# Kernel tuning notes

Measured on AMD Instinct MI355X. Metric: run time of the kernel, lower is better.

The kernel has to match this reference:

```python
import jax, jax.numpy as jnp
import numpy as np
from jax import lax

K = 9
CENTER = K // 2
EXTEND = 1.0
EPS = 1e-5
GROUPS = 16  # out_ch // 4


def conv2d(x, w, b, stride, padding):
    y = lax.conv_general_dilated(x, w, window_strides=stride, padding=padding,
                                 dimension_numbers=('NCHW', 'OIHW', 'NCHW'))
    return y + b[None, :, None, None]


def setup_inputs() -> dict:
    key = jax.random.key(0)
    ks = jax.random.split(key, 9)
    B, C, Wd, Hd, OUT = 8, 64, 128, 128, 64
    f = jax.random.normal(ks[0], (B, C, Wd, Hd), jnp.float32)
    w_off = jax.random.normal(ks[1], (2 * K, C, 3, 3), jnp.float32) * 0.05
    b_off = jax.random.normal(ks[2], (2 * K,), jnp.float32) * 0.05
    bn_gamma = 1.0 + 0.1 * jax.random.normal(ks[3], (2 * K,), jnp.float32)
    bn_beta = 0.1 * jax.random.normal(ks[4], (2 * K,), jnp.float32)
    w_dsc = jax.random.normal(ks[5], (OUT, C, K, 1), jnp.float32) * 0.05
    b_dsc = jax.random.normal(ks[6], (OUT,), jnp.float32) * 0.05
    gn_gamma = 1.0 + 0.1 * jax.random.normal(ks[7], (OUT,), jnp.float32)
    gn_beta = 0.1 * jax.random.normal(ks[8], (OUT,), jnp.float32)
    return {'f': f, 'w_off': w_off, 'b_off': b_off, 'bn_gamma': bn_gamma,
            'bn_beta': bn_beta, 'w_dsc': w_dsc, 'b_dsc': b_dsc,
            'gn_gamma': gn_gamma, 'gn_beta': gn_beta}


def _forward(f, w_off, b_off, bn_gamma, bn_beta, w_dsc, b_dsc, gn_gamma, gn_beta):
    B, C, Wd, Hd = f.shape  # module names: width=shape[2], height=shape[3]
    dt = f.dtype

    # offset branch: conv3x3 -> BatchNorm (training mode, batch stats) -> tanh
    off = conv2d(f, w_off, b_off, (1, 1), 'SAME')
    mu = off.mean(axis=(0, 2, 3), keepdims=True)
    var = off.var(axis=(0, 2, 3), keepdims=True)
    off = (off - mu) / jnp.sqrt(var + EPS)
    off = off * bn_gamma[None, :, None, None] + bn_beta[None, :, None, None]
    off = jnp.tanh(off)

    y_off = off[:, :K]  # [B,K,Wd,Hd]; x_off (off[:, K:]) unused for morph=0

    # cumulative offset scan from the center point (morph=0).
    # NOTE: endpoints 0 and K-1 keep detached raw offsets (torch detach().clone()).
    raw0 = lax.stop_gradient(y_off)
    offn = [None] * K
    offn[CENTER] = jnp.zeros_like(y_off[:, 0])
    for i in range(1, CENTER):
        offn[CENTER + i] = offn[CENTER + i - 1] + y_off[:, CENTER + i]
        offn[CENTER - i] = offn[CENTER - i + 1] + y_off[:, CENTER - i]
    offn[0] = raw0[:, 0]
    offn[K - 1] = raw0[:, K - 1]
    offn = jnp.stack(offn, axis=1)  # [B,K,Wd,Hd]

    # coordinate grids: y indexes the width axis, x the height axis
    y_new = jnp.arange(Wd, dtype=dt)[None, None, :, None] + offn * EXTEND  # [B,K,Wd,Hd]
    x_new = ((jnp.arange(K, dtype=dt) - CENTER)[None, :, None, None]
             + jnp.arange(Hd, dtype=dt)[None, None, None, :])  # [1,K,1,Hd]
    x_new = jnp.broadcast_to(x_new, (B, K, Wd, Hd))

    # layout [B, K*Wd, Hd] via (B,K,Wd,Hd) -> (B,Wd,K,Hd)
    y_s = jnp.transpose(y_new, (0, 2, 1, 3)).reshape(B, K * Wd * Hd)
    x_s = jnp.transpose(x_new, (0, 2, 1, 3)).reshape(B, K * Wd * Hd)

    # bilinear interpolation (clamped corner indices, unclamped y/x in weights)
    y0 = jnp.floor(y_s).astype(jnp.int32)
    x0 = jnp.floor(x_s).astype(jnp.int32)
    y0c = jnp.clip(y0, 0, Wd - 1)
    y1c = jnp.clip(y0 + 1, 0, Wd - 1)
    x0c = jnp.clip(x0, 0, Hd - 1)
    x1c = jnp.clip(x0 + 1, 0, Hd - 1)

    feat = jnp.transpose(f, (0, 2, 3, 1)).reshape(B, Wd * Hd, C)

    def gather(yi, xi):
        idx = (yi * Hd + xi)[:, :, None]  # [B,N,1]
        return jnp.take_along_axis(feat, idx, axis=1)  # [B,N,C]

    va0 = gather(y0c, x0c)
    vc0 = gather(y0c, x1c)
    va1 = gather(y1c, x0c)
    vc1 = gather(y1c, x1c)

    y0f, y1f = y0c.astype(dt), y1c.astype(dt)
    x0f, x1f = x0c.astype(dt), x1c.astype(dt)
    wa = ((y1f - y_s) * (x1f - x_s))[:, :, None]
    wb = ((y1f - y_s) * (x_s - x0f))[:, :, None]
    wc = ((y_s - y0f) * (x1f - x_s))[:, :, None]
    wd = ((y_s - y0f) * (x_s - x0f))[:, :, None]

    out = va0 * wa + vc0 * wb + va1 * wc + vc1 * wd  # [B,N,C]
    deformed = jnp.transpose(out.reshape(B, K * Wd, Hd, C), (0, 3, 1, 2))  # [B,C,K*Wd,Hd]

    # strided conv over the K snake points -> [B,OUT,Wd,Hd]
    x = conv2d(deformed, w_dsc, b_dsc, (K, 1), 'VALID')

    # GroupNorm + ReLU
    OUT = x.shape[1]
    xg = x.reshape(B, GROUPS, -1)
    gmu = xg.mean(axis=-1, keepdims=True)
    gvar = xg.var(axis=-1, keepdims=True)
    xg = (xg - gmu) / jnp.sqrt(gvar + EPS)
    x = xg.reshape(x.shape) * gn_gamma[None, :, None, None] + gn_beta[None, :, None, None]
    return jax.nn.relu(x)


def reference(f, w_off, b_off, bn_gamma, bn_beta, w_dsc, b_dsc, gn_gamma, gn_beta):
    return _forward(f, w_off, b_off, bn_gamma, bn_beta, w_dsc, b_dsc, gn_gamma, gn_beta)
```

## Files before the change

### kernel.cpp

```cpp
#include <hip/hip_runtime.h>

#define B_   8
#define C_   64
#define W_   128
#define H_   128
#define K_   9
#define OUT_ 64
#define NPIX (B_*W_*H_)
#define EPS_ 1e-5f

typedef __attribute__((ext_vector_type(8))) short bf16x8;
typedef __attribute__((ext_vector_type(4))) float f32x4;

#define FEATBF_OFF  0
#define XPRE_OFF    4194304
#define OFFPRE_OFF  8388608
#define OFFH_OFF    9568256
#define WT_OFF      14286848
#define WP_OFF      14305280
#define BNSTATS_OFF 14310464
#define GSTATS_OFF  14310500
#define STATS_BYTES ((18+18+256+256)*sizeof(float))

__device__ __forceinline__ unsigned pack2bf(float a, float b) {
    union { float f; unsigned u; } ua, ub;
    ua.f = a; ub.f = b;
    unsigned x = ua.u, y = ub.u;
    x += 0x7fffu + ((x >> 16) & 1u);
    y += 0x7fffu + ((y >> 16) & 1u);
    return (x >> 16) | (y & 0xffff0000u);
}
__device__ __forceinline__ float bflo(unsigned u) {
    union { unsigned u; float f; } v; v.u = u << 16; return v.f;
}
__device__ __forceinline__ float bfhi(unsigned u) {
    union { unsigned u; float f; } v; v.u = u & 0xffff0000u; return v.f;
}

__global__ __launch_bounds__(256) void k_nhwc(const float* __restrict__ f,
                                              unsigned short* __restrict__ featbf) {
    __shared__ float tile[64][65];
    int bid = blockIdx.x;
    int ht = bid & 1;
    int w  = (bid >> 1) & 127;
    int b  = bid >> 8;
    int t  = threadIdx.x;
    int lh = t & 63;
    int c0 = (t >> 6) * 16;
    const float* fp = f + (((b*64)*128 + w)*128) + ht*64 + lh;
#pragma unroll
    for (int i = 0; i < 16; i++) {
        int c = c0 + i;
        tile[c][lh] = fp[c*16384];
    }
    __syncthreads();
    int lc = t & 63;
    int h0 = (t >> 6) * 16;
    unsigned short* obf = featbf + ((size_t)((b*128 + w)*128) + ht*64)*64 + lc;
#pragma unroll
    for (int i = 0; i < 16; i++) {
        int hr = h0 + i;
        union { float f; unsigned u; } v; v.f = tile[lc][hr];
        unsigned x = v.u + 0x7fffu + ((v.u >> 16) & 1u);
        obf[(size_t)hr*64] = (unsigned short)(x >> 16);
    }
}

__global__ void k_wprep(const float* __restrict__ w_dsc, unsigned short* __restrict__ wTbf,
                        const float* __restrict__ w_off, float* __restrict__ wP) {
    int bid = blockIdx.x;
    if (bid < 144) {
        int i = bid*256 + threadIdx.x;
        if (i >= 9*64*64) return;
        int c = i & 63;
        int o = (i >> 6) & 63;
        int k = i >> 12;
        union { float f; unsigned u; } v;
        v.f = w_dsc[(o*64 + c)*9 + k];
        unsigned x = v.u + 0x7fffu + ((v.u >> 16) & 1u);
        wTbf[i] = (unsigned short)(x >> 16);
    } else {
        int i = (bid-144)*256 + threadIdx.x;
        if (i >= 64*81) return;
        int c    = i / 81;
        int rem  = i % 81;
        int dw   = rem / 27;
        int rem2 = rem % 27;
        int ck   = rem2 / 3;
        int dh   = rem2 % 3;
        wP[i] = w_off[ck*576 + c*9 + dw*3 + dh];
    }
}

__global__ __launch_bounds__(128) void k_conv_off(const float* __restrict__ f,
                                                  const float* __restrict__ wP,
                                                  float* __restrict__ off_half) {
    int t   = threadIdx.x;
    int bid = blockIdx.x;
    int b   = bid & 7;
    int w   = (bid >> 3) & 127;
    int cq  = bid >> 10;
    int h   = t;

    float em = (h == 0)   ? 0.f : 1.f;
    float ep = (h == 127) ? 0.f : 1.f;

    const float* fb = f + (size_t)b*1048576 + (size_t)(cq*16)*16384 + (size_t)w*128;
    const float* wb = wP + cq*16*81;

    float acc[9];
#pragma unroll
    for (int ck = 0; ck < 9; ck++) acc[ck] = 0.f;

#pragma unroll 4
    for (int c = 0; c < 16; c++) {
        const float* p  = fb + c*16384;
        const float* wc = wb + c*81;
#pragma unroll
        for (int dw = -1; dw <= 1; dw++) {
            int wy = w + dw;
            if ((unsigned)wy < 128u) {
                const float* q = p + dw*128;
                float v1 = q[h];
                float v0 = __shfl_up(v1, 1);
                float v2 = __shfl_down(v1, 1);
                if (t == 64) v0 = q[63];
                if (t == 63) v2 = q[64];
                v0 *= em; v2 *= ep;
                const float* ww = wc + (dw+1)*27;
#pragma unroll
                for (int ck = 0; ck < 9; ck++)
                    acc[ck] += v0*ww[ck*3] + v1*ww[ck*3+1] + v2*ww[ck*3+2];
            }
        }
    }

    float* dst = off_half + (size_t)cq*1179648;
    int pixoff = (w << 7) + h;
#pragma unroll
    for (int ck = 0; ck < 9; ck++)
        dst[((b*9 + ck) << 14) + pixoff] = acc[ck];
}

__global__ __launch_bounds__(256) void k_bn_stats(const float* __restrict__ off_half,
                                                  float* __restrict__ off_pre,
                                                  float* __restrict__ bnstats) {
    __shared__ float wred[4][2];
    int bid = blockIdx.x;
    int b  = bid / 36;
    int rem = bid % 36;
    int ck = rem / 4;
    int wq = rem % 4;
    int t  = threadIdx.x;
    int base4 = (((b*9+ck) << 14) + wq*4096) >> 2;

    const float4* h0 = (const float4*)off_half;
    const float4* h1 = (const float4*)(off_half + 1179648);
    const float4* h2 = (const float4*)(off_half + 2359296);
    const float4* h3 = (const float4*)(off_half + 3538944);
    float4* op = (float4*)off_pre;

    float s = 0.f, q = 0.f;
#pragma unroll
    for (int i = 0; i < 4; i++) {
        int idx = base4 + t + i*256;
        float4 a = h0[idx], bb = h1[idx], cc = h2[idx], dd = h3[idx];
        float4 v;
        v.x = (a.x + bb.x) + (cc.x + dd.x);
        v.y = (a.y + bb.y) + (cc.y + dd.y);
        v.z = (a.z + bb.z) + (cc.z + dd.z);
        v.w = (a.w + bb.w) + (cc.w + dd.w);
        op[idx] = v;
        s += v.x + v.y + v.z + v.w;
        q += v.x*v.x + v.y*v.y + v.z*v.z + v.w*v.w;
    }
    for (int off = 32; off; off >>= 1) {
        s += __shfl_down(s, off);
        q += __shfl_down(q, off);
    }
    if ((t & 63) == 0) { wred[t >> 6][0] = s; wred[t >> 6][1] = q; }
    __syncthreads();
    if (t == 0) atomicAdd(&bnstats[ck*2],   wred[0][0]+wred[1][0]+wred[2][0]+wred[3][0]);
    if (t == 1) atomicAdd(&bnstats[ck*2+1], wred[0][1]+wred[1][1]+wred[2][1]+wred[3][1]);
}

__global__ __launch_bounds__(256) void k_sample_dsc(const unsigned short* __restrict__ featbf,
                                                    const float* __restrict__ off_pre,
                                                    const float* __restrict__ bnstats,
                                                    const float* __restrict__ bn_gamma,
                                                    const float* __restrict__ bn_beta,
                                                    const unsigned short* __restrict__ wTbf,
                                                    const float* __restrict__ b_dsc,
                                                    unsigned short* __restrict__ xprebf,
                                                    float* __restrict__ gstats) {
    __shared__ __align__(16) unsigned char lds_samp[2][64*128];
    __shared__ __align__(16) unsigned char lds_wk[2][64*128];
    __shared__ float ynew[9][64];
    __shared__ float red[16][2];
    __shared__ float bnab[18];

    int t = threadIdx.x;
    int bid = blockIdx.x;
    int b = bid & 7, w = (bid >> 3) & 127, mh = bid >> 10;
    int hbase = mh * 64;

    if (t < 9) {
        float n    = (float)NPIX;
        float mean = bnstats[t*2] / n;
        float var  = bnstats[t*2+1] / n - mean*mean;
        float A    = bn_gamma[t] / sqrtf(var + EPS_);
        bnab[t*2]   = A;
        bnab[t*2+1] = bn_beta[t] - mean * A;
    }
    if (t < 16) { red[t][0] = 0.f; red[t][1] = 0.f; }
    __syncthreads();

    if (t < 64) {
        int h = hbase + t;
        float y[9];
#pragma unroll
        for (int ck = 0; ck < 9; ck++) {
            float v = off_pre[((b*9+ck) << 14) + (w << 7) + h];
            y[ck] = tanhf(bnab[ck*2]*v + bnab[ck*2+1]);
        }
        float ofn[9];
        ofn[4] = 0.f;
        ofn[5] = y[5]; ofn[6] = y[5]+y[6]; ofn[7] = y[5]+y[6]+y[7];
        ofn[3] = y[3]; ofn[2] = y[3]+y[2]; ofn[1] = y[3]+y[2]+y[1];
        ofn[0] = y[0]; ofn[8] = y[8];
#pragma unroll
        for (int k = 0; k < 9; k++) ynew[k][t] = (float)w + ofn[k];
    }
    __syncthreads();

    f32x4 acc[4];
#pragma unroll
    for (int ni = 0; ni < 4; ni++) {
        acc[ni][0] = 0.f; acc[ni][1] = 0.f; acc[ni][2] = 0.f; acc[ni][3] = 0.f;
    }

    int lane = t & 63, wv = t >> 6;
    int m0 = wv * 16;
    int lm = lane & 15, lk = lane >> 4;
    int hsl = t >> 2;
    int cq  = t & 3;
    const unsigned short* pbase = featbf + ((size_t)b << 20);

    uint4 sa0, sa1, sb0, sb1, wv0, wv1;
    float twa = 0.f, twc = 0.f;
    bool valid = false;

    {
        int hg = hbase + hsl;
        int x0 = 0 - 4 + hg;
        valid = (unsigned)x0 < 127u;
        if (valid) {
            float ys = ynew[0][hsl];
            int y0  = (int)floorf(ys);
            int y0c = min(max(y0, 0), 127), y1c = min(max(y0+1, 0), 127);
            twa = (float)y1c - ys; twc = ys - (float)y0c;
            const uint4* p0 = (const uint4*)(pbase + (y0c*128 + x0)*64) + cq*2;
            const uint4* p1 = (const uint4*)(pbase + (y1c*128 + x0)*64) + cq*2;
            sa0 = p0[0]; sa1 = p0[1];
            sb0 = p1[0]; sb1 = p1[1];
        }
        const uint4* src = (const uint4*)wTbf;
        wv0 = src[t]; wv1 = src[t + 256];
    }
    {
        unsigned char* dst = lds_samp[0] + hsl*128;
        int bcol0 = cq * 32;
        uint4 u0 = make_uint4(0,0,0,0), u1 = make_uint4(0,0,0,0);
        if (valid) {
            u0.x = pack2bf(bflo(sa0.x)*twa + bflo(sb0.x)*twc, bfhi(sa0.x)*twa + bfhi(sb0.x)*twc);
            u0.y = pack2bf(bflo(sa0.y)*twa + bflo(sb0.y)*twc, bfhi(sa0.y)*twa + bfhi(sb0.y)*twc);
            u0.z = pack2bf(bflo(sa0.z)*twa + bflo(sb0.z)*twc, bfhi(sa0.z)*twa + bfhi(sb0.z)*twc);
            u0.w = pack2bf(bflo(sa0.w)*twa + bflo(sb0.w)*twc, bfhi(sa0.w)*twa + bfhi(sb0.w)*twc);
            u1.x = pack2bf(bflo(sa1.x)*twa + bflo(sb1.x)*twc, bfhi(sa1.x)*twa + bfhi(sb1.x)*twc);
            u1.y = pack2bf(bflo(sa1.y)*twa + bflo(sb1.y)*twc, bfhi(sa1.y)*twa + bfhi(sb1.y)*twc);
            u1.z = pack2bf(bflo(sa1.z)*twa + bflo(sb1.z)*twc, bfhi(sa1.z)*twa + bfhi(sb1.z)*twc);
            u1.w = pack2bf(bflo(sa1.w)*twa + bflo(sb1.w)*twc, bfhi(sa1.w)*twa + bfhi(sb1.w)*twc);
        }
        *(uint4*)(dst + ((bcol0     ) ^ ((hsl & 7) << 4))) = u0;
        *(uint4*)(dst + ((bcol0 + 16) ^ ((hsl & 7) << 4))) = u1;
#pragma unroll
        for (int i = 0; i < 2; i++) {
            int ci = t + i*256;
            uint4 v = (i == 0) ? wv0 : wv1;
            int o  = ci >> 3;
            int cb = (ci & 7) << 4;
            *(uint4*)(lds_wk[0] + o*128 + (cb ^ ((o & 7) << 4))) = v;
        }
    }
    __syncthreads();

    for (int k = 0; k < 9; k++) {
        int cur = k & 1, nxt = cur ^ 1;

        if (k < 8) {
            int hg = hbase + hsl;
            int x0 = (k+1) - 4 + hg;
            valid = (unsigned)x0 < 127u;
            if (valid) {
                float ys = ynew[k+1][hsl];
                int y0  = (int)floorf(ys);
                int y0c = min(max(y0, 0), 127), y1c = min(max(y0+1, 0), 127);
                twa = (float)y1c - ys; twc = ys - (float)y0c;
                const uint4* p0 = (const uint4*)(pbase + (y0c*128 + x0)*64) + cq*2;
                const uint4* p1 = (const uint4*)(pbase + (y1c*128 + x0)*64) + cq*2;
                sa0 = p0[0]; sa1 = p0[1];
                sb0 = p1[0]; sb1 = p1[1];
            }
            const uint4* src = (const uint4*)(wTbf + ((k+1) << 12));
            wv0 = src[t]; wv1 = src[t + 256];
        }

#pragma unroll
        for (int ks = 0; ks < 2; ks++) {
            bf16x8 af, bfr[4];
            {
                int hl = m0 + lm;
                af = *(const bf16x8*)(lds_samp[cur] + hl*128 + ((ks*64 + lk*16) ^ ((hl & 7) << 4)));
            }
#pragma unroll
            for (int ni = 0; ni < 4; ni++) {
                int o = ni*16 + lm;
                bfr[ni] = *(const bf16x8*)(lds_wk[cur] + o*128 + ((ks*64 + lk*16) ^ ((o & 7) << 4)));
            }
#pragma unroll
            for (int ni = 0; ni < 4; ni++)
                acc[ni] = __builtin_amdgcn_mfma_f32_16x16x32_bf16(af, bfr[ni], acc[ni], 0, 0, 0);
        }

        if (k < 8) {
            unsigned char* dst = lds_samp[nxt] + hsl*128;
            int bcol0 = cq * 32;
            uint4 u0 = make_uint4(0,0,0,0), u1 = make_uint4(0,0,0,0);
            if (valid) {
                u0.x = pack2bf(bflo(sa0.x)*twa + bflo(sb0.x)*twc, bfhi(sa0.x)*twa + bfhi(sb0.x)*twc);
                u0.y = pack2bf(bflo(sa0.y)*twa + bflo(sb0.y)*twc, bfhi(sa0.y)*twa + bfhi(sb0.y)*twc);
                u0.z = pack2bf(bflo(sa0.z)*twa + bflo(sb0.z)*twc, bfhi(sa0.z)*twa + bfhi(sb0.z)*twc);
                u0.w = pack2bf(bflo(sa0.w)*twa + bflo(sb0.w)*twc, bfhi(sa0.w)*twa + bfhi(sb0.w)*twc);
                u1.x = pack2bf(bflo(sa1.x)*twa + bflo(sb1.x)*twc, bfhi(sa1.x)*twa + bfhi(sb1.x)*twc);
                u1.y = pack2bf(bflo(sa1.y)*twa + bflo(sb1.y)*twc, bfhi(sa1.y)*twa + bfhi(sb1.y)*twc);
                u1.z = pack2bf(bflo(sa1.z)*twa + bflo(sb1.z)*twc, bfhi(sa1.z)*twa + bfhi(sb1.z)*twc);
                u1.w = pack2bf(bflo(sa1.w)*twa + bflo(sb1.w)*twc, bfhi(sa1.w)*twa + bfhi(sb1.w)*twc);
            }
            *(uint4*)(dst + ((bcol0     ) ^ ((hsl & 7) << 4))) = u0;
            *(uint4*)(dst + ((bcol0 + 16) ^ ((hsl & 7) << 4))) = u1;
#pragma unroll
            for (int i = 0; i < 2; i++) {
                int ci = t + i*256;
                uint4 v = (i == 0) ? wv0 : wv1;
                int o  = ci >> 3;
                int cb = (ci & 7) << 4;
                *(uint4*)(lds_wk[nxt] + o*128 + (cb ^ ((o & 7) << 4))) = v;
            }
            __syncthreads();
        }
    }

#pragma unroll
    for (int ni = 0; ni < 4; ni++) {
        int o = ni*16 + lm;
        float bias = b_dsc[o];
        float4 r;
        r.x = acc[ni][0] + bias;
        r.y = acc[ni][1] + bias;
        r.z = acc[ni][2] + bias;
        r.w = acc[ni][3] + bias;
        float s1 = r.x + r.y + r.z + r.w;
        float s2 = r.x*r.x + r.y*r.y + r.z*r.z + r.w*r.w;
        int hg = hbase + m0 + lk*4;
        uint2 u2;
        u2.x = pack2bf(r.x, r.y);
        u2.y = pack2bf(r.z, r.w);
        *(uint2*)(xprebf + (((b*64 + o) << 14) + (w << 7) + hg)) = u2;

        s1 += __shfl_xor(s1, 1);  s1 += __shfl_xor(s1, 2);
        s1 += __shfl_xor(s1, 16); s1 += __shfl_xor(s1, 32);
        s2 += __shfl_xor(s2, 1);  s2 += __shfl_xor(s2, 2);
        s2 += __shfl_xor(s2, 16); s2 += __shfl_xor(s2, 32);
        if (lk == 0 && (lm & 3) == 0) {
            atomicAdd(&red[ni*4 + (lm >> 2)][0], s1);
            atomicAdd(&red[ni*4 + (lm >> 2)][1], s2);
        }
    }
    __syncthreads();
    if (t < 16) {
        atomicAdd(&gstats[(b*16 + t)*2],   red[t][0]);
        atomicAdd(&gstats[(b*16 + t)*2+1], red[t][1]);
    }
}

__global__ __launch_bounds__(256) void k_gn_apply(const unsigned short* __restrict__ xprebf,
                                                  const float* __restrict__ gstats,
                                                  const float* __restrict__ gn_gamma,
                                                  const float* __restrict__ gn_beta,
                                                  float* __restrict__ out) {
    int i8  = blockIdx.x*256 + threadIdx.x;
    int idx = i8 * 8;
    int o = (idx >> 14) & 63;
    int b = idx >> 20;
    int g = o >> 2;
    float n    = 65536.f;
    float mean = gstats[(b*16+g)*2] / n;
    float var  = gstats[(b*16+g)*2+1] / n - mean*mean;
    float istd = 1.0f / sqrtf(var + EPS_);
    float ga = gn_gamma[o] * istd;
    float be = gn_beta[o] - mean * ga;
    uint4 v = *(const uint4*)(xprebf + idx);
    float4 r0, r1;
    r0.x = fmaxf(bflo(v.x)*ga + be, 0.f);
    r0.y = fmaxf(bfhi(v.x)*ga + be, 0.f);
    r0.z = fmaxf(bflo(v.y)*ga + be, 0.f);
    r0.w = fmaxf(bfhi(v.y)*ga + be, 0.f);
    r1.x = fmaxf(bflo(v.z)*ga + be, 0.f);
    r1.y = fmaxf(bfhi(v.z)*ga + be, 0.f);
    r1.z = fmaxf(bflo(v.w)*ga + be, 0.f);
    r1.w = fmaxf(bfhi(v.w)*ga + be, 0.f);
    *(float4*)(out + idx)     = r0;
    *(float4*)(out + idx + 4) = r1;
}

extern "C" void kernel_launch(void* const* d_in, const int* in_sizes, int n_in,
                              void* d_out, int out_size, void* d_ws, size_t ws_size,
                              hipStream_t stream) {
    const float* f        = (const float*)d_in[0];
    const float* w_off    = (const float*)d_in[1];
    const float* bn_gamma = (const float*)d_in[3];
    const float* bn_beta  = (const float*)d_in[4];
    const float* w_dsc    = (const float*)d_in[5];
    const float* b_dsc    = (const float*)d_in[6];
    const float* gn_gamma = (const float*)d_in[7];
    const float* gn_beta  = (const float*)d_in[8];

    float* ws      = (float*)d_ws;
    unsigned short* featbf = (unsigned short*)(ws + FEATBF_OFF);
    unsigned short* xprebf = (unsigned short*)(ws + XPRE_OFF);
    float* off_pre = ws + OFFPRE_OFF;
    float* off_half= ws + OFFH_OFF;
    unsigned short* wTbf = (unsigned short*)(ws + WT_OFF);
    float* wP      = ws + WP_OFF;
    float* bnstats = ws + BNSTATS_OFF;
    float* gstats  = ws + GSTATS_OFF;

    hipMemsetAsync(bnstats, 0, STATS_BYTES, stream);

    k_nhwc<<<2048, 256, 0, stream>>>(f, featbf);
    k_wprep<<<165, 256, 0, stream>>>(w_dsc, wTbf, w_off, wP);
    k_conv_off<<<4096, 128, 0, stream>>>(f, wP, off_half);
    k_bn_stats<<<288, 256, 0, stream>>>(off_half, off_pre, bnstats);
    k_sample_dsc<<<2048, 256, 0, stream>>>(featbf, off_pre, bnstats, bn_gamma, bn_beta,
                                           wTbf, b_dsc, xprebf, gstats);
    k_gn_apply<<<4096, 256, 0, stream>>>(xprebf, gstats, gn_gamma, gn_beta, (float*)d_out);
}
```

Measured before the change: 125.5 us.

## Build sampled A fragments in registers instead of staging through LDS

```diff
diff --git a/kernel.cpp b/kernel.cpp
--- a/kernel.cpp
+++ b/kernel.cpp
@@ -193,7 +193,6 @@
                                                     const float* __restrict__ b_dsc,
                                                     unsigned short* __restrict__ xprebf,
                                                     float* __restrict__ gstats) {
-    __shared__ __align__(16) unsigned char lds_samp[2][64*128];
     __shared__ __align__(16) unsigned char lds_wk[2][64*128];
     __shared__ float ynew[9][64];
     __shared__ float red[16][2];
@@ -231,6 +230,19 @@
 #pragma unroll
         for (int k = 0; k < 9; k++) ynew[k][t] = (float)w + ofn[k];
     }
+
+    {
+        const uint4* src = (const uint4*)wTbf;
+        uint4 a = src[t], c = src[t + 256];
+#pragma unroll
+        for (int i = 0; i < 2; i++) {
+            int ci = t + i*256;
+            uint4 v = (i == 0) ? a : c;
+            int o  = ci >> 3;
+            int cb = (ci & 7) << 4;
+            *(uint4*)(lds_wk[0] + o*128 + (cb ^ ((o & 7) << 4))) = v;
+        }
+    }
     __syncthreads();
 
     f32x4 acc[4];
@@ -242,86 +254,77 @@
     int lane = t & 63, wv = t >> 6;
     int m0 = wv * 16;
     int lm = lane & 15, lk = lane >> 4;
-    int hsl = t >> 2;
-    int cq  = t & 3;
+    int hl = m0 + lm;
+    int hg = hbase + hl;
     const unsigned short* pbase = featbf + ((size_t)b << 20);
 
-    uint4 sa0, sa1, sb0, sb1, wv0, wv1;
+    uint4 s00, s01, s10, s11;
     float twa = 0.f, twc = 0.f;
-    bool valid = false;
+    bool valid;
 
     {
-        int hg = hbase + hsl;
         int x0 = 0 - 4 + hg;
         valid = (unsigned)x0 < 127u;
         if (valid) {
-            float ys = ynew[0][hsl];
+            float ys = ynew[0][hl];
             int y0  = (int)floorf(ys);
             int y0c = min(max(y0, 0), 127), y1c = min(max(y0+1, 0), 127);
             twa = (float)y1c - ys; twc = ys - (float)y0c;
-            const uint4* p0 = (const uint4*)(pbase + (y0c*128 + x0)*64) + cq*2;
-            const uint4* p1 = (const uint4*)(pbase + (y1c*128 + x0)*64) + cq*2;
-            sa0 = p0[0]; sa1 = p0[1];
-            sb0 = p1[0]; sb1 = p1[1];
-        }
-        const uint4* src = (const uint4*)wTbf;
-        wv0 = src[t]; wv1 = src[t + 256];
-    }
-    {
-        unsigned char* dst = lds_samp[0] + hsl*128;
-        int bcol0 = cq * 32;
-        uint4 u0 = make_uint4(0,0,0,0), u1 = make_uint4(0,0,0,0);
-        if (valid) {
-            u0.x = pack2bf(bflo(sa0.x)*twa + bflo(sb0.x)*twc, bfhi(sa0.x)*twa + bfhi(sb0.x)*twc);
-            u0.y = pack2bf(bflo(sa0.y)*twa + bflo(sb0.y)*twc, bfhi(sa0.y)*twa + bfhi(sb0.y)*twc);
-            u0.z = pack2bf(bflo(sa0.z)*twa + bflo(sb0.z)*twc, bfhi(sa0.z)*twa + bfhi(sb0.z)*twc);
-            u0.w = pack2bf(bflo(sa0.w)*twa + bflo(sb0.w)*twc, bfhi(sa0.w)*twa + bfhi(sb0.w)*twc);
-            u1.x = pack2bf(bflo(sa1.x)*twa + bflo(sb1.x)*twc, bfhi(sa1.x)*twa + bfhi(sb1.x)*twc);
-            u1.y = pack2bf(bflo(sa1.y)*twa + bflo(sb1.y)*twc, bfhi(sa1.y)*twa + bfhi(sb1.y)*twc);
-            u1.z = pack2bf(bflo(sa1.z)*twa + bflo(sb1.z)*twc, bfhi(sa1.z)*twa + bfhi(sb1.z)*twc);
-            u1.w = pack2bf(bflo(sa1.w)*twa + bflo(sb1.w)*twc, bfhi(sa1.w)*twa + bfhi(sb1.w)*twc);
-        }
-        *(uint4*)(dst + ((bcol0     ) ^ ((hsl & 7) << 4))) = u0;
-        *(uint4*)(dst + ((bcol0 + 16) ^ ((hsl & 7) << 4))) = u1;
-#pragma unroll
-        for (int i = 0; i < 2; i++) {
-            int ci = t + i*256;
-            uint4 v = (i == 0) ? wv0 : wv1;
-            int o  = ci >> 3;
-            int cb = (ci & 7) << 4;
-            *(uint4*)(lds_wk[0] + o*128 + (cb ^ ((o & 7) << 4))) = v;
-        }
-    }
-    __syncthreads();
-
+            const unsigned short* r0 = pbase + (y0c*128 + x0)*64 + lk*8;
+            const unsigned short* r1 = pbase + (y1c*128 + x0)*64 + lk*8;
+            s00 = *(const uint4*)r0;  s01 = *(const uint4*)(r0 + 32);
+            s10 = *(const uint4*)r1;  s11 = *(const uint4*)(r1 + 32);
+        }
+    }
+
+#pragma unroll
     for (int k = 0; k < 9; k++) {
-        int cur = k & 1, nxt = cur ^ 1;
-
+        int cur = k & 1;
+
+        uint4 wv0, wv1;
         if (k < 8) {
-            int hg = hbase + hsl;
+            const uint4* src = (const uint4*)(wTbf + ((k+1) << 12));
+            wv0 = src[t]; wv1 = src[t + 256];
+        }
+
+        bf16x8 af[2];
+        {
+            union { uint4 u; bf16x8 v; } r0, r1;
+            if (valid) {
+                r0.u.x = pack2bf(bflo(s00.x)*twa + bflo(s10.x)*twc, bfhi(s00.x)*twa + bfhi(s10.x)*twc);
+                r0.u.y = pack2bf(bflo(s00.y)*twa + bflo(s10.y)*twc, bfhi(s00.y)*twa + bfhi(s10.y)*twc);
+                r0.u.z = pack2bf(bflo(s00.z)*twa + bflo(s10.z)*twc, bfhi(s00.z)*twa + bfhi(s10.z)*twc);
+                r0.u.w = pack2bf(bflo(s00.w)*twa + bflo(s10.w)*twc, bfhi(s00.w)*twa + bfhi(s10.w)*twc);
+                r1.u.x = pack2bf(bflo(s01.x)*twa + bflo(s11.x)*twc, bfhi(s01.x)*twa + bfhi(s11.x)*twc);
+                r1.u.y = pack2bf(bflo(s01.y)*twa + bflo(s11.y)*twc, bfhi(s01.y)*twa + bfhi(s11.y)*twc);
+                r1.u.z = pack2bf(bflo(s01.z)*twa + bflo(s11.z)*twc, bfhi(s01.z)*twa + bfhi(s11.z)*twc);
+                r1.u.w = pack2bf(bflo(s01.w)*twa + bflo(s11.w)*twc, bfhi(s01.w)*twa + bfhi(s11.w)*twc);
+            } else {
+                r0.u = make_uint4(0,0,0,0);
+                r1.u = make_uint4(0,0,0,0);
+            }
+            af[0] = r0.v;
+            af[1] = r1.v;
+        }
+
+        if (k < 8) {
             int x0 = (k+1) - 4 + hg;
             valid = (unsigned)x0 < 127u;
             if (valid) {
-                float ys = ynew[k+1][hsl];
+                float ys = ynew[k+1][hl];
                 int y0  = (int)floorf(ys);
                 int y0c = min(max(y0, 0), 127), y1c = min(max(y0+1, 0), 127);
                 twa = (float)y1c - ys; twc = ys - (float)y0c;
-                const uint4* p0 = (const uint4*)(pbase + (y0c*128 + x0)*64) + cq*2;
-                const uint4* p1 = (const uint4*)(pbase + (y1c*128 + x0)*64) + cq*2;
-                sa0 = p0[0]; sa1 = p0[1];
-                sb0 = p1[0]; sb1 = p1[1];
+                const unsigned short* r0 = pbase + (y0c*128 + x0)*64 + lk*8;
+                const unsigned short* r1 = pbase + (y1c*128 + x0)*64 + lk*8;
+                s00 = *(const uint4*)r0;  s01 = *(const uint4*)(r0 + 32);
+                s10 = *(const uint4*)r1;  s11 = *(const uint4*)(r1 + 32);
             }
-            const uint4* src = (const uint4*)(wTbf + ((k+1) << 12));
-            wv0 = src[t]; wv1 = src[t + 256];
         }
 
 #pragma unroll
         for (int ks = 0; ks < 2; ks++) {
-            bf16x8 af, bfr[4];
-            {
-                int hl = m0 + lm;
-                af = *(const bf16x8*)(lds_samp[cur] + hl*128 + ((ks*64 + lk*16) ^ ((hl & 7) << 4)));
-            }
+            bf16x8 bfr[4];
 #pragma unroll
             for (int ni = 0; ni < 4; ni++) {
                 int o = ni*16 + lm;
@@ -329,32 +332,17 @@
             }
 #pragma unroll
             for (int ni = 0; ni < 4; ni++)
-                acc[ni] = __builtin_amdgcn_mfma_f32_16x16x32_bf16(af, bfr[ni], acc[ni], 0, 0, 0);
+                acc[ni] = __builtin_amdgcn_mfma_f32_16x16x32_bf16(af[ks], bfr[ni], acc[ni], 0, 0, 0);
         }
 
         if (k < 8) {
-            unsigned char* dst = lds_samp[nxt] + hsl*128;
-            int bcol0 = cq * 32;
-            uint4 u0 = make_uint4(0,0,0,0), u1 = make_uint4(0,0,0,0);
-            if (valid) {
-                u0.x = pack2bf(bflo(sa0.x)*twa + bflo(sb0.x)*twc, bfhi(sa0.x)*twa + bfhi(sb0.x)*twc);
-                u0.y = pack2bf(bflo(sa0.y)*twa + bflo(sb0.y)*twc, bfhi(sa0.y)*twa + bfhi(sb0.y)*twc);
-                u0.z = pack2bf(bflo(sa0.z)*twa + bflo(sb0.z)*twc, bfhi(sa0.z)*twa + bfhi(sb0.z)*twc);
-                u0.w = pack2bf(bflo(sa0.w)*twa + bflo(sb0.w)*twc, bfhi(sa0.w)*twa + bfhi(sb0.w)*twc);
-                u1.x = pack2bf(bflo(sa1.x)*twa + bflo(sb1.x)*twc, bfhi(sa1.x)*twa + bfhi(sb1.x)*twc);
-                u1.y = pack2bf(bflo(sa1.y)*twa + bflo(sb1.y)*twc, bfhi(sa1.y)*twa + bfhi(sb1.y)*twc);
-                u1.z = pack2bf(bflo(sa1.z)*twa + bflo(sb1.z)*twc, bfhi(sa1.z)*twa + bfhi(sb1.z)*twc);
-                u1.w = pack2bf(bflo(sa1.w)*twa + bflo(sb1.w)*twc, bfhi(sa1.w)*twa + bfhi(sb1.w)*twc);
-            }
-            *(uint4*)(dst + ((bcol0     ) ^ ((hsl & 7) << 4))) = u0;
-            *(uint4*)(dst + ((bcol0 + 16) ^ ((hsl & 7) << 4))) = u1;
 #pragma unroll
             for (int i = 0; i < 2; i++) {
                 int ci = t + i*256;
                 uint4 v = (i == 0) ? wv0 : wv1;
                 int o  = ci >> 3;
                 int cb = (ci & 7) << 4;
-                *(uint4*)(lds_wk[nxt] + o*128 + (cb ^ ((o & 7) << 4))) = v;
+                *(uint4*)(lds_wk[cur ^ 1] + o*128 + (cb ^ ((o & 7) << 4))) = v;
             }
             __syncthreads();
         }
@@ -371,11 +359,11 @@
         r.w = acc[ni][3] + bias;
         float s1 = r.x + r.y + r.z + r.w;
         float s2 = r.x*r.x + r.y*r.y + r.z*r.z + r.w*r.w;
-        int hg = hbase + m0 + lk*4;
+        int hgo = hbase + m0 + lk*4;
         uint2 u2;
         u2.x = pack2bf(r.x, r.y);
         u2.y = pack2bf(r.z, r.w);
-        *(uint2*)(xprebf + (((b*64 + o) << 14) + (w << 7) + hg)) = u2;
+        *(uint2*)(xprebf + (((b*64 + o) << 14) + (w << 7) + hgo)) = u2;
 
         s1 += __shfl_xor(s1, 1);  s1 += __shfl_xor(s1, 2);
         s1 += __shfl_xor(s1, 16); s1 += __shfl_xor(s1, 32);
```

Measured after the change: 139.8 us. 11.4% more time.
